# Kernel optimization log

Measured on AMD Instinct MI355X. Metric: run time of the kernel, lower is better.

The kernel has to match this reference:

```python
import jax, jax.numpy as jnp
import numpy as np

EPS = 1e-6

def _mlp3(x, Wa, ba, Wb, bb, Wc, bc):
    h = jax.nn.relu(x @ Wa + ba)
    h = jax.nn.relu(h @ Wb + bb)
    return h @ Wc + bc

def setup_inputs() -> dict:
    key = jax.random.key(0)
    ks = jax.random.split(key, 16)
    B, D, C, N = 1024, 1024, 128, 100000
    s = 0.02  # weight scale
    return {
        "query": jax.random.normal(ks[0], (B, D), jnp.float32),
        "W1": jax.random.normal(ks[1], (D, D // 2), jnp.float32) * s,
        "b1": jnp.zeros((D // 2,), jnp.float32),
        "W2": jax.random.normal(ks[2], (D // 2, D // 4), jnp.float32) * s,
        "b2": jnp.zeros((D // 4,), jnp.float32),
        "W3": jax.random.normal(ks[3], (D // 4, C), jnp.float32) * s,
        "b3": jnp.zeros((C,), jnp.float32),
        "keys": jax.random.normal(ks[4], (N, C), jnp.float32),
        "values": jax.random.normal(ks[5], (N, C), jnp.float32),
        "D1w": jax.random.normal(ks[6], (C, D // 4), jnp.float32) * s,
        "D1b": jnp.zeros((D // 4,), jnp.float32),
        "D2w": jax.random.normal(ks[7], (D // 4, D // 2), jnp.float32) * s,
        "D2b": jnp.zeros((D // 2,), jnp.float32),
        "D3w": jax.random.normal(ks[8], (D // 2, D), jnp.float32) * s,
        "D3b": jnp.zeros((D,), jnp.float32),
        "k": 5,
    }

def reference(query, W1, b1, W2, b2, W3, b3, keys, values,
              D1w, D1b, D2w, D2b, D3w, D3b, k):
    # Compress query (FAISS path detaches, so stop_gradient is faithful)
    cq = _mlp3(query, W1, b1, W2, b2, W3, b3)          # [B, C]
    cq = jax.lax.stop_gradient(cq)
    keys_c = jax.lax.stop_gradient(keys)
    vals = jax.lax.stop_gradient(values)               # stored values were .detach()ed
    # Brute-force squared-L2 distances (IndexFlatL2 returns squared L2): [B, N]
    d2 = (jnp.sum(cq * cq, axis=1, keepdims=True)
          + jnp.sum(keys_c * keys_c, axis=1)[None, :]
          - 2.0 * cq @ keys_c.T)
    neg_d, idx = jax.lax.top_k(-d2, k)                 # k nearest, ascending distance
    dist = -neg_d                                      # [B, k]
    w = 1.0 / (dist + EPS)
    w = w / jnp.sum(w, axis=1, keepdims=True)          # [B, k]
    gathered = vals[idx]                               # [B, k, C]
    weighted = jnp.einsum('bk,bkc->bc', w, gathered)   # [B, C]
    retrieved = _mlp3(weighted, D1w, D1b, D2w, D2b, D3w, D3b)  # [B, D]
    confidence = 1.0 / (dist[:, 0] + EPS)              # [B]
    return retrieved, confidence
```

## Files before the change

### kernel.cpp

```cpp
#include <hip/hip_runtime.h>
#include <hip/hip_bf16.h>

#define NKEYS  100000
#define NCH    128
#define CHK    832
#define TPC    13
#define KPAD   (NCH * CHK)
#define NTILE  (KPAD / 64)
#define BQ     1024
#define EPS_F  1e-6f
#define NCAND  (NCH * 3)
#define BIGF   1e30f

typedef __attribute__((ext_vector_type(8))) short bf16x8;
typedef __attribute__((ext_vector_type(4))) float f32x4;

__device__ __forceinline__ void gl_lds16(const uint4* g, uint4* l) {
    __builtin_amdgcn_global_load_lds((const __attribute__((address_space(1))) void*)g,
                                     (__attribute__((address_space(3))) void*)l, 16, 0, 0);
}
__device__ __forceinline__ unsigned umn(unsigned a, unsigned b) { return a < b ? a : b; }
__device__ __forceinline__ unsigned umx(unsigned a, unsigned b) { return a > b ? a : b; }
__device__ __forceinline__ ushort bf16bits(float v) {
    __hip_bfloat16 h = __float2bfloat16(v);
    return *(ushort*)&h;
}

__device__ __forceinline__ void ins3u(unsigned (&m)[3], unsigned u) {
    unsigned v1 = umn(m[2], u);
    m[2] = umx(m[1], v1);
    unsigned v2 = umn(m[1], v1);
    m[1] = umx(m[0], v2);
    m[0] = umn(m[0], v2);
}

__device__ __forceinline__ void ins5(float (&d)[5], int (&ix)[5], float nd, int ni) {
    if (nd < d[4]) {
        d[4] = nd; ix[4] = ni;
#pragma unroll
        for (int p = 4; p > 0; --p) {
            if (d[p] < d[p - 1]) {
                float td = d[p]; d[p] = d[p - 1]; d[p - 1] = td;
                int   ti = ix[p]; ix[p] = ix[p - 1]; ix[p - 1] = ti;
            }
        }
    }
}

__device__ __forceinline__ void wT_panel(const float* __restrict__ W, uint4* __restrict__ Wimg,
                                         int K, int N, int ctile, int p) {
    const int npan = K >> 6;
#pragma unroll
    for (int it = 0; it < 2; ++it) {
        int c = it * 256 + threadIdx.x;
        int l15 = c & 15, quad = (c >> 4) & 3, s = (c >> 6) & 1, ct = c >> 7;
        int n = ctile * 64 + ct * 16 + l15;
        int k = p * 64 + s * 32 + quad * 8;
        ushort h[8];
#pragma unroll
        for (int j = 0; j < 8; ++j) h[j] = bf16bits(W[(size_t)(k + j) * N + n]);
        Wimg[((size_t)ctile * npan + p) * 512 + c] =
            make_uint4((uint)h[0] | ((uint)h[1] << 16), (uint)h[2] | ((uint)h[3] << 16),
                       (uint)h[4] | ((uint)h[5] << 16), (uint)h[6] | ((uint)h[7] << 16));
    }
}

__global__ __launch_bounds__(256)
void cvt_keys_w(const float* __restrict__ keys, uint4* __restrict__ img,
                float* __restrict__ kk, float* __restrict__ khalf,
                const float* __restrict__ D1w, const float* __restrict__ D2w,
                const float* __restrict__ D3w, uint4* __restrict__ I1,
                uint4* __restrict__ I2, uint4* __restrict__ I3) {
    if (blockIdx.x >= NTILE) {
        int b = blockIdx.x - NTILE;
        if (b < 8)       { wT_panel(D1w, I1, 128, 256,  b >> 1, b & 1); }
        else if (b < 40) { b -= 8;  wT_panel(D2w, I2, 256, 512,  b >> 2, b & 3); }
        else             { b -= 40; wT_panel(D3w, I3, 512, 1024, b >> 3, b & 7); }
        return;
    }
    const int tid = threadIdx.x;
    const int r = tid >> 2, s = tid & 3;
    const int tile = blockIdx.x;
    const int n = tile * 64 + r;
    const int ct = r >> 4, l15 = r & 15;
    const bool live = (n < NKEYS);
    const float* kp = keys + (size_t)n * 128 + s * 32;
    float ss = 0.f;
    uint4 out[4];
#pragma unroll
    for (int q = 0; q < 4; ++q) {
        float4 a = make_float4(0.f, 0.f, 0.f, 0.f), b = a;
        if (live) { a = *(const float4*)(kp + q * 8); b = *(const float4*)(kp + q * 8 + 4); }
        ss += a.x * a.x + a.y * a.y + a.z * a.z + a.w * a.w
            + b.x * b.x + b.y * b.y + b.z * b.z + b.w * b.w;
        float v[8] = {a.x, a.y, a.z, a.w, b.x, b.y, b.z, b.w};
        ushort h[8];
#pragma unroll
        for (int j = 0; j < 8; ++j) h[j] = bf16bits(v[j]);
        out[q] = make_uint4((uint)h[0] | ((uint)h[1] << 16), (uint)h[2] | ((uint)h[3] << 16),
                            (uint)h[4] | ((uint)h[5] << 16), (uint)h[6] | ((uint)h[7] << 16));
    }
    ss += __shfl_xor(ss, 1, 64);
    ss += __shfl_xor(ss, 2, 64);
    if (s == 0) {
        kk[n]    = live ? ss : BIGF;
        khalf[n] = live ? -0.5f * ss : -BIGF;
    }
#pragma unroll
    for (int q = 0; q < 4; ++q)
        img[(size_t)tile * 1024 + ((ct * 4 + s) * 4 + q) * 16 + l15] = out[q];
}

__global__ __launch_bounds__(256)
void prep(const float* __restrict__ A, ushort* __restrict__ Ax,
          const float* __restrict__ W, uint4* __restrict__ Wimg) {
    const int b = blockIdx.x;
    if (b < 1024) {
        const int row = b;
        const int i = threadIdx.x * 4;
        float4 v = *(const float4*)&A[(size_t)row * 1024 + i];
        float x[4] = {v.x, v.y, v.z, v.w};
        ushort h[4], l[4];
#pragma unroll
        for (int j = 0; j < 4; ++j) {
            __hip_bfloat16 hb = __float2bfloat16(x[j]);
            h[j] = *(ushort*)&hb;
            l[j] = bf16bits(x[j] - __bfloat162float(hb));
        }
        ushort* o = Ax + (size_t)row * 3072;
        *(ushort4*)&o[i]        = make_ushort4(h[0], h[1], h[2], h[3]);
        *(ushort4*)&o[1024 + i] = make_ushort4(l[0], l[1], l[2], l[3]);
        *(ushort4*)&o[2048 + i] = make_ushort4(h[0], h[1], h[2], h[3]);
    } else {
        const int idx = b - 1024;
        const int ctile = idx / 48, p = idx % 48;
        const int part = p >> 4, psrc = p & 15;
#pragma unroll
        for (int it = 0; it < 2; ++it) {
            int c = it * 256 + threadIdx.x;
            int l15 = c & 15, quad = (c >> 4) & 3, s = (c >> 6) & 1, ct = c >> 7;
            int n = ctile * 64 + ct * 16 + l15;
            int k = psrc * 64 + s * 32 + quad * 8;
            ushort h[8];
#pragma unroll
            for (int j = 0; j < 8; ++j) {
                float w = W[(size_t)(k + j) * 512 + n];
                __hip_bfloat16 hb = __float2bfloat16(w);
                if (part < 2) h[j] = *(ushort*)&hb;
                else h[j] = bf16bits(w - __bfloat162float(hb));
            }
            Wimg[((size_t)ctile * 48 + p) * 512 + c] =
                make_uint4((uint)h[0] | ((uint)h[1] << 16), (uint)h[2] | ((uint)h[3] << 16),
                           (uint)h[4] | ((uint)h[5] << 16), (uint)h[6] | ((uint)h[7] << 16));
        }
    }
}

__global__ __launch_bounds__(256)
void bgemm_part(const ushort* __restrict__ Abf, const uint4* __restrict__ Wimg,
                float* __restrict__ P, int M, int N, int K, int ppz) {
    __shared__ uint4 pan[2][512];
    const int tid = threadIdx.x;
    const int wv = tid >> 6, ln = tid & 63;
    const int quad = ln >> 4, l15 = ln & 15;
    const int n0 = blockIdx.x * 64;
    const int m0 = blockIdx.y * 128 + wv * 32;
    const int ctile = blockIdx.x, npanT = K >> 6;
    const int p0 = blockIdx.z * ppz;
    f32x4 acc[2][4];
#pragma unroll
    for (int s = 0; s < 2; ++s)
#pragma unroll
        for (int c = 0; c < 4; ++c) acc[s][c] = (f32x4){0.f, 0.f, 0.f, 0.f};

#pragma unroll
    for (int it = 0; it < 2; ++it)
        gl_lds16(&Wimg[((size_t)ctile * npanT + p0) * 512 + it * 256 + wv * 64 + ln],
                 &pan[0][it * 256 + wv * 64]);
    __syncthreads();

    for (int pp = 0; pp < ppz; ++pp) {
        const int p = p0 + pp;
        const int b = pp & 1;
        if (pp + 1 < ppz) {
#pragma unroll
            for (int it = 0; it < 2; ++it)
                gl_lds16(&Wimg[((size_t)ctile * npanT + p + 1) * 512 + it * 256 + wv * 64 + ln],
                         &pan[b ^ 1][it * 256 + wv * 64]);
        }
        const ushort* arow = Abf + (size_t)(m0 + l15) * K + p * 64 + quad * 8;
        bf16x8 afA[2], afB[2];
#pragma unroll
        for (int s = 0; s < 2; ++s) {
            afA[s] = *(const bf16x8*)(arow + s * 32);
            afB[s] = *(const bf16x8*)(arow + (size_t)16 * K + s * 32);
        }
#pragma unroll
        for (int ct = 0; ct < 4; ++ct)
#pragma unroll
            for (int s = 0; s < 2; ++s) {
                bf16x8 bfr = *(const bf16x8*)&pan[b][((ct * 2 + s) * 4 + quad) * 16 + l15];
                acc[0][ct] = __builtin_amdgcn_mfma_f32_16x16x32_bf16(afA[s], bfr, acc[0][ct], 0, 0, 0);
                acc[1][ct] = __builtin_amdgcn_mfma_f32_16x16x32_bf16(afB[s], bfr, acc[1][ct], 0, 0, 0);
            }
        __syncthreads();
    }

    P += (size_t)blockIdx.z * M * N;
#pragma unroll
    for (int ct = 0; ct < 4; ++ct) {
        const int col = n0 + ct * 16 + l15;
#pragma unroll
        for (int set = 0; set < 2; ++set)
#pragma unroll
            for (int r = 0; r < 4; ++r)
                P[(size_t)(m0 + set * 16 + quad * 4 + r) * N + col] = acc[set][ct][r];
    }
}

template <int NP>
__global__ __launch_bounds__(256)
void sgemm_part(const float* __restrict__ A, const float* __restrict__ abias,
                const float* __restrict__ W, float* __restrict__ P,
                int M, int N, int K, int kslice, int MNpart) {
    __shared__ float As[16][68];
    __shared__ float Bs[16][64];
    const int tid = threadIdx.x;
    const int tx = tid & 15, ty = tid >> 4;
    const int m0 = blockIdx.y * 64, n0 = blockIdx.x * 64;
    const int kb = blockIdx.z * kslice, ke = kb + kslice;
    float acc[4][4] = {};
    for (int k0 = kb; k0 < ke; k0 += 16) {
        {
            int m = tid >> 2, k4 = (tid & 3) * 4;
            const float* ap = &A[(size_t)(m0 + m) * K + k0 + k4];
            float4 a = *(const float4*)ap;
            if (NP > 0) {
#pragma unroll
                for (int z = 1; z < NP; ++z) {
                    float4 v = *(const float4*)(ap + (size_t)z * MNpart);
                    a.x += v.x; a.y += v.y; a.z += v.z; a.w += v.w;
                }
                float4 b = *(const float4*)&abias[k0 + k4];
                a.x = fmaxf(a.x + b.x, 0.f); a.y = fmaxf(a.y + b.y, 0.f);
                a.z = fmaxf(a.z + b.z, 0.f); a.w = fmaxf(a.w + b.w, 0.f);
            }
            As[k4 + 0][m] = a.x; As[k4 + 1][m] = a.y;
            As[k4 + 2][m] = a.z; As[k4 + 3][m] = a.w;
        }
        {
            int k = tid >> 4, n4 = (tid & 15) * 4;
            *(float4*)&Bs[k][n4] = *(const float4*)&W[(size_t)(k0 + k) * N + n0 + n4];
        }
        __syncthreads();
#pragma unroll
        for (int kkk = 0; kkk < 16; ++kkk) {
            float4 a4 = *(const float4*)&As[kkk][ty * 4];
            float4 b4 = *(const float4*)&Bs[kkk][tx * 4];
            float av[4] = {a4.x, a4.y, a4.z, a4.w};
            float bv[4] = {b4.x, b4.y, b4.z, b4.w};
#pragma unroll
            for (int i = 0; i < 4; ++i)
#pragma unroll
                for (int j = 0; j < 4; ++j)
                    acc[i][j] = fmaf(av[i], bv[j], acc[i][j]);
        }
        __syncthreads();
    }
    P += (size_t)blockIdx.z * M * N;
#pragma unroll
    for (int i = 0; i < 4; ++i)
        *(float4*)&P[(size_t)(m0 + ty * 4 + i) * N + n0 + tx * 4] =
            make_float4(acc[i][0], acc[i][1], acc[i][2], acc[i][3]);
}

__global__ __launch_bounds__(128)
void layer3_full(const float* __restrict__ partB, const float* __restrict__ b2,
                 const float* __restrict__ W3, const float* __restrict__ b3,
                 float* __restrict__ cq, ushort* __restrict__ qbf,
                 float* __restrict__ qq) {
    __shared__ float h2s[256];
    __shared__ float red[2];
    const int row = blockIdx.x, c = threadIdx.x;
#pragma unroll
    for (int u = 0; u < 2; ++u) {
        const int k = c + u * 128;
        float v = 0.f;
#pragma unroll
        for (int z = 0; z < 4; ++z) v += partB[(size_t)z * (BQ * 256) + row * 256 + k];
        h2s[k] = fmaxf(v + b2[k], 0.f);
    }
    __syncthreads();
    float a0 = 0.f, a1 = 0.f, a2 = 0.f, a3 = 0.f;
#pragma unroll 4
    for (int k = 0; k < 256; k += 4) {
        a0 = fmaf(h2s[k + 0], W3[(size_t)(k + 0) * 128 + c], a0);
        a1 = fmaf(h2s[k + 1], W3[(size_t)(k + 1) * 128 + c], a1);
        a2 = fmaf(h2s[k + 2], W3[(size_t)(k + 2) * 128 + c], a2);
        a3 = fmaf(h2s[k + 3], W3[(size_t)(k + 3) * 128 + c], a3);
    }
    const float out = (a0 + a1) + (a2 + a3) + b3[c];
    cq[(size_t)row * 128 + c] = out;
    qbf[(size_t)row * 128 + c] = bf16bits(out);
    float s = out * out;
#pragma unroll
    for (int off = 32; off > 0; off >>= 1) s += __shfl_down(s, off, 64);
    if ((c & 63) == 0) red[c >> 6] = s;
    __syncthreads();
    if (c == 0) qq[row] = red[0] + red[1];
}

__global__ __launch_bounds__(512, 4)
void screen_topk(const ushort* __restrict__ qbf, const uint4* __restrict__ img,
                 const float* __restrict__ khalf, int* __restrict__ cand_i) {
    __shared__ uint4 buf[2][1024];
    __shared__ float kls[CHK];
    const int tid = threadIdx.x;
    const int wv = tid >> 6, ln = tid & 63;
    const int quad = ln >> 4, l15 = ln & 15;
    const int m0 = blockIdx.y * 256 + wv * 32;
    const int c0 = blockIdx.x * CHK;
    const int t0 = blockIdx.x * TPC;

    bf16x8 afA[4], afB[4];
    {
        const ushort* qa = qbf + (size_t)(m0 + l15) * 128 + quad * 8;
#pragma unroll
        for (int s = 0; s < 4; ++s) {
            afA[s] = *(const bf16x8*)(qa + 32 * s);
            afB[s] = *(const bf16x8*)(qa + 16 * 128 + 32 * s);
        }
    }
    for (int i = tid; i < CHK; i += 512) kls[i] = khalf[c0 + i];

    unsigned mA[4][3], mB[4][3];
#pragma unroll
    for (int r = 0; r < 4; ++r)
#pragma unroll
        for (int p = 0; p < 3; ++p) { mA[r][p] = 0xFFFFFFFFu; mB[r][p] = 0xFFFFFFFFu; }

#pragma unroll
    for (int it = 0; it < 2; ++it)
        gl_lds16(&img[(size_t)t0 * 1024 + it * 512 + wv * 64 + ln],
                 &buf[0][it * 512 + wv * 64]);
    __syncthreads();

    for (int t = 0; t < TPC; ++t) {
        const int b = t & 1;
        if (t + 1 < TPC) {
#pragma unroll
            for (int it = 0; it < 2; ++it)
                gl_lds16(&img[(size_t)(t0 + t + 1) * 1024 + it * 512 + wv * 64 + ln],
                         &buf[b ^ 1][it * 512 + wv * 64]);
        }
#pragma unroll
        for (int ct = 0; ct < 4; ++ct) {
            const int nl = t * 64 + ct * 16 + l15;
            const float kh = kls[nl];
            f32x4 a0 = {kh, kh, kh, kh}, a1 = {kh, kh, kh, kh};
#pragma unroll
            for (int s = 0; s < 4; ++s) {
                bf16x8 bfr = *(const bf16x8*)&buf[b][(ct * 4 + s) * 64 + ln];
                a0 = __builtin_amdgcn_mfma_f32_16x16x32_bf16(afA[s], bfr, a0, 0, 0, 0);
                a1 = __builtin_amdgcn_mfma_f32_16x16x32_bf16(afB[s], bfr, a1, 0, 0, 0);
            }
#pragma unroll
            for (int r = 0; r < 4; ++r) {
                ins3u(mA[r], (__float_as_uint(a0[r]) & 0xFFFFF800u) | (unsigned)nl);
                ins3u(mB[r], (__float_as_uint(a1[r]) & 0xFFFFF800u) | (unsigned)nl);
            }
        }
        __syncthreads();
    }

#pragma unroll
    for (int set = 0; set < 2; ++set) {
#pragma unroll
        for (int r = 0; r < 4; ++r) {
            unsigned m[3];
#pragma unroll
            for (int p = 0; p < 3; ++p) m[p] = set ? mB[r][p] : mA[r][p];
#pragma unroll
            for (int st = 1; st <= 8; st <<= 1) {
                unsigned o[3];
#pragma unroll
                for (int p = 0; p < 3; ++p) o[p] = (unsigned)__shfl_xor((int)m[p], st, 64);
#pragma unroll
                for (int p = 0; p < 3; ++p) ins3u(m, o[p]);
            }
            if (l15 == 0) {
                const int row = m0 + set * 16 + quad * 4 + r;
#pragma unroll
                for (int p = 0; p < 3; ++p)
                    cand_i[((size_t)row * NCH + blockIdx.x) * 3 + p] = c0 + (int)(m[p] & 0x7FFu);
            }
        }
    }
}

__global__ __launch_bounds__(512)
void rerank_gather(const int* __restrict__ cand_i, const float* __restrict__ cq,
                   const float* __restrict__ keysf, const float* __restrict__ qq,
                   const float* __restrict__ kk, const float* __restrict__ values,
                   ushort* __restrict__ wbf, float* __restrict__ conf_out) {
    __shared__ __align__(16) float qs[128];
    __shared__ float ed[NCAND];
    __shared__ int   ei[NCAND];
    __shared__ float w5[5];
    __shared__ int   s5[5];
    __shared__ float confs;
    const int row = blockIdx.x, tid = threadIdx.x;
    const int ln = tid & 63;
    const int qd = tid >> 4;
    const int l15 = tid & 15;
    if (tid < 128) qs[tid] = cq[(size_t)row * 128 + tid];
    for (int c = tid; c < NCAND; c += 512) ei[c] = cand_i[(size_t)row * NCAND + c];
    __syncthreads();
    const float4 qa = *(const float4*)&qs[l15 * 8];
    const float4 qb = *(const float4*)&qs[l15 * 8 + 4];
    const float qqr = qq[row];
#pragma unroll 3
    for (int it = 0; it < (NCAND + 31) / 32; ++it) {
        const int c = qd + it * 32;
        if (c < NCAND) {
            const int idx = ei[c];
            const int idc = idx < NKEYS ? idx : NKEYS - 1;
            const float* kp = &keysf[(size_t)idc * 128 + l15 * 8];
            const float4 ka = *(const float4*)kp;
            const float4 kb = *(const float4*)(kp + 4);
            float dot = qa.x * ka.x + qa.y * ka.y + qa.z * ka.z + qa.w * ka.w
                      + qb.x * kb.x + qb.y * kb.y + qb.z * kb.z + qb.w * kb.w;
            dot += __shfl_xor(dot, 1, 64);
            dot += __shfl_xor(dot, 2, 64);
            dot += __shfl_xor(dot, 4, 64);
            dot += __shfl_xor(dot, 8, 64);
            if (l15 == 0) ed[c] = qqr + kk[idx] - 2.0f * dot;
        }
    }
    __syncthreads();
    if (tid < 64) {
        float bd[5]; int bi[5];
#pragma unroll
        for (int p = 0; p < 5; ++p) { bd[p] = BIGF; bi[p] = 0; }
        for (int c = ln; c < NCAND; c += 64) ins5(bd, bi, ed[c], ei[c]);
#pragma unroll
        for (int m = 1; m <= 32; m <<= 1) {
            float od[5]; int oi[5];
#pragma unroll
            for (int p = 0; p < 5; ++p) {
                od[p] = __shfl_xor(bd[p], m, 64);
                oi[p] = __shfl_xor(bi[p], m, 64);
            }
#pragma unroll
            for (int p = 0; p < 5; ++p) ins5(bd, bi, od[p], oi[p]);
        }
        if (ln == 0) {
            float ww[5]; float s = 0.f;
#pragma unroll
            for (int p = 0; p < 5; ++p) { ww[p] = 1.0f / (bd[p] + EPS_F); s += ww[p]; }
#pragma unroll
            for (int p = 0; p < 5; ++p) { w5[p] = ww[p] / s; s5[p] = bi[p]; }
            confs = 1.0f / (bd[0] + EPS_F);
        }
    }
    __syncthreads();
    if (tid < 128) {
        float acc = 0.f;
#pragma unroll
        for (int p = 0; p < 5; ++p) acc += w5[p] * values[(size_t)s5[p] * 128 + tid];
        wbf[(size_t)row * 128 + tid] = bf16bits(acc);
    }
    if (tid == 0) conf_out[row] = confs;
}

template <int RELU, int OUTF32>
__global__ __launch_bounds__(256)
void bgemm_bias(const ushort* __restrict__ Abf, const uint4* __restrict__ Wimg,
                const float* __restrict__ bias, void* __restrict__ Cout,
                int M, int N, int K) {
    __shared__ uint4 pan[2][512];
    const int tid = threadIdx.x;
    const int wv = tid >> 6, ln = tid & 63;
    const int quad = ln >> 4, l15 = ln & 15;
    const int n0 = blockIdx.x * 64;
    const int m0 = blockIdx.y * 128 + wv * 32;
    const int ctile = blockIdx.x, npan = K >> 6;
    f32x4 acc[2][4];
#pragma unroll
    for (int s = 0; s < 2; ++s)
#pragma unroll
        for (int c = 0; c < 4; ++c) acc[s][c] = (f32x4){0.f, 0.f, 0.f, 0.f};

#pragma unroll
    for (int it = 0; it < 2; ++it)
        gl_lds16(&Wimg[(size_t)ctile * npan * 512 + it * 256 + wv * 64 + ln],
                 &pan[0][it * 256 + wv * 64]);
    __syncthreads();

    for (int p = 0; p < npan; ++p) {
        const int b = p & 1;
        if (p + 1 < npan) {
#pragma unroll
            for (int it = 0; it < 2; ++it)
                gl_lds16(&Wimg[((size_t)ctile * npan + p + 1) * 512 + it * 256 + wv * 64 + ln],
                         &pan[b ^ 1][it * 256 + wv * 64]);
        }
        const ushort* arow = Abf + (size_t)(m0 + l15) * K + p * 64 + quad * 8;
        bf16x8 afA[2], afB[2];
#pragma unroll
        for (int s = 0; s < 2; ++s) {
            afA[s] = *(const bf16x8*)(arow + s * 32);
            afB[s] = *(const bf16x8*)(arow + (size_t)16 * K + s * 32);
        }
#pragma unroll
        for (int ct = 0; ct < 4; ++ct)
#pragma unroll
            for (int s = 0; s < 2; ++s) {
                bf16x8 bfr = *(const bf16x8*)&pan[b][((ct * 2 + s) * 4 + quad) * 16 + l15];
                acc[0][ct] = __builtin_amdgcn_mfma_f32_16x16x32_bf16(afA[s], bfr, acc[0][ct], 0, 0, 0);
                acc[1][ct] = __builtin_amdgcn_mfma_f32_16x16x32_bf16(afB[s], bfr, acc[1][ct], 0, 0, 0);
            }
        __syncthreads();
    }

#pragma unroll
    for (int ct = 0; ct < 4; ++ct) {
        const int col = n0 + ct * 16 + l15;
        const float bv = bias[col];
#pragma unroll
        for (int set = 0; set < 2; ++set)
#pragma unroll
            for (int r = 0; r < 4; ++r) {
                float v = acc[set][ct][r] + bv;
                if (RELU) v = fmaxf(v, 0.f);
                const int row = m0 + set * 16 + quad * 4 + r;
                if (OUTF32) ((float*)Cout)[(size_t)row * N + col] = v;
                else        ((ushort*)Cout)[(size_t)row * N + col] = bf16bits(v);
            }
    }
}

extern "C" void kernel_launch(void* const* d_in, const int* in_sizes, int n_in,
                              void* d_out, int out_size, void* d_ws, size_t ws_size,
                              hipStream_t stream) {
    const float* query  = (const float*)d_in[0];
    const float* W1     = (const float*)d_in[1];
    const float* b1     = (const float*)d_in[2];
    const float* W2     = (const float*)d_in[3];
    const float* b2     = (const float*)d_in[4];
    const float* W3     = (const float*)d_in[5];
    const float* b3     = (const float*)d_in[6];
    const float* keys   = (const float*)d_in[7];
    const float* values = (const float*)d_in[8];
    const float* D1w    = (const float*)d_in[9];
    const float* D1b    = (const float*)d_in[10];
    const float* D2w    = (const float*)d_in[11];
    const float* D2b    = (const float*)d_in[12];
    const float* D3w    = (const float*)d_in[13];
    const float* D3b    = (const float*)d_in[14];
    float* out = (float*)d_out;

    float*  ws    = (float*)d_ws;
    float*  kk    = ws;
    float*  khalf = ws + 106496;
    float*  qq    = ws + 212992;
    float*  cq    = ws + 214016;
    ushort* qbf   = (ushort*)(ws + 345088);
    int*    cand  = (int*)(ws + 410624);
    uint4*  Wimg1 = (uint4*)(ws + 803840);
    uint4*  Wimg2 = (uint4*)(ws + 820224);
    uint4*  Wimg3 = (uint4*)(ws + 885760);
    float*  R     = ws + 1147904;
    ushort* xbig  = (ushort*)R;
    uint4*  W1img = (uint4*)(R + 1572864);
    float*  partA = R + 2359296;
    float*  partB = R + 5505024;
    uint4*  img   = (uint4*)R;
    ushort* wbf   = (ushort*)R;
    ushort* h3bf  = (ushort*)(R + 65536);
    ushort* h4bf  = (ushort*)(R + 196608);
    float*  conf  = out + 1024 * 1024;

    prep<<<1408, 256, 0, stream>>>(query, xbig, W1, W1img);
    bgemm_part<<<dim3(8, 8, 6), 256, 0, stream>>>(xbig, W1img, partA, 1024, 512, 3072, 8);
    sgemm_part<6><<<dim3(4, 16, 4), 256, 0, stream>>>(partA, b1, W2, partB, 1024, 256, 512, 128, 1024 * 512);
    layer3_full<<<1024, 128, 0, stream>>>(partB, b2, W3, b3, cq, qbf, qq);
    cvt_keys_w<<<NTILE + 168, 256, 0, stream>>>(keys, img, kk, khalf,
                                                D1w, D2w, D3w, Wimg1, Wimg2, Wimg3);
    screen_topk<<<dim3(NCH, BQ / 256), 512, 0, stream>>>(qbf, img, khalf, cand);
    rerank_gather<<<BQ, 512, 0, stream>>>(cand, cq, keys, qq, kk, values, wbf, conf);
    bgemm_bias<1, 0><<<dim3(4, 8),  256, 0, stream>>>(wbf,  Wimg1, D1b, h3bf, 1024, 256,  128);
    bgemm_bias<1, 0><<<dim3(8, 8),  256, 0, stream>>>(h3bf, Wimg2, D2b, h4bf, 1024, 512,  256);
    bgemm_bias<0, 1><<<dim3(16, 8), 256, 0, stream>>>(h4bf, Wimg3, D3b, out,  1024, 1024, 512);

    (void)in_sizes; (void)n_in; (void)out_size; (void)ws_size;
}
```

Before: 283.3 us.

## Rebalance screen_topk to 64 rows per wave and shrink decoder GEMM row tiles

screen_topk now runs 256 threads per block, with each wave owning 64 query rows (4 MFMA sets) instead of 32. Each key fragment read from LDS is reused across twice as many MFMAs, which cuts LDS traffic per MFMA, but each thread holds more top-3 registers and occupancy may drop. The decoder bgemm_bias kernels move the other way: each wave computes 16 rows instead of 32, giving twice as many blocks to fill more CUs on these small GEMMs, at the cost of less reuse of the weight panel.

Result: no change. 284.1 us (+0.3%).

```diff
diff --git a/kernel.cpp b/kernel.cpp
--- a/kernel.cpp
+++ b/kernel.cpp
@@ -310,7 +310,7 @@
     if (c == 0) qq[row] = red[0] + red[1];
 }
 
-__global__ __launch_bounds__(512, 4)
+__global__ __launch_bounds__(256)
 void screen_topk(const ushort* __restrict__ qbf, const uint4* __restrict__ img,
                  const float* __restrict__ khalf, int* __restrict__ cand_i) {
     __shared__ uint4 buf[2][1024];
@@ -318,68 +318,71 @@
     const int tid = threadIdx.x;
     const int wv = tid >> 6, ln = tid & 63;
     const int quad = ln >> 4, l15 = ln & 15;
-    const int m0 = blockIdx.y * 256 + wv * 32;
+    const int m0 = blockIdx.y * 256 + wv * 64;
     const int c0 = blockIdx.x * CHK;
     const int t0 = blockIdx.x * TPC;
 
-    bf16x8 afA[4], afB[4];
-    {
-        const ushort* qa = qbf + (size_t)(m0 + l15) * 128 + quad * 8;
-#pragma unroll
-        for (int s = 0; s < 4; ++s) {
-            afA[s] = *(const bf16x8*)(qa + 32 * s);
-            afB[s] = *(const bf16x8*)(qa + 16 * 128 + 32 * s);
-        }
-    }
-    for (int i = tid; i < CHK; i += 512) kls[i] = khalf[c0 + i];
-
-    unsigned mA[4][3], mB[4][3];
-#pragma unroll
-    for (int r = 0; r < 4; ++r)
-#pragma unroll
-        for (int p = 0; p < 3; ++p) { mA[r][p] = 0xFFFFFFFFu; mB[r][p] = 0xFFFFFFFFu; }
-
-#pragma unroll
-    for (int it = 0; it < 2; ++it)
-        gl_lds16(&img[(size_t)t0 * 1024 + it * 512 + wv * 64 + ln],
-                 &buf[0][it * 512 + wv * 64]);
+    bf16x8 af[4][4];
+#pragma unroll
+    for (int set = 0; set < 4; ++set) {
+        const ushort* qa = qbf + (size_t)(m0 + set * 16 + l15) * 128 + quad * 8;
+#pragma unroll
+        for (int s = 0; s < 4; ++s) af[set][s] = *(const bf16x8*)(qa + 32 * s);
+    }
+    for (int i = tid; i < CHK; i += 256) kls[i] = khalf[c0 + i];
+
+    unsigned mm[4][4][3];
+#pragma unroll
+    for (int set = 0; set < 4; ++set)
+#pragma unroll
+        for (int r = 0; r < 4; ++r)
+#pragma unroll
+            for (int p = 0; p < 3; ++p) mm[set][r][p] = 0xFFFFFFFFu;
+
+#pragma unroll
+    for (int it = 0; it < 4; ++it)
+        gl_lds16(&img[(size_t)t0 * 1024 + it * 256 + wv * 64 + ln],
+                 &buf[0][it * 256 + wv * 64]);
     __syncthreads();
 
     for (int t = 0; t < TPC; ++t) {
         const int b = t & 1;
         if (t + 1 < TPC) {
 #pragma unroll
-            for (int it = 0; it < 2; ++it)
-                gl_lds16(&img[(size_t)(t0 + t + 1) * 1024 + it * 512 + wv * 64 + ln],
-                         &buf[b ^ 1][it * 512 + wv * 64]);
+            for (int it = 0; it < 4; ++it)
+                gl_lds16(&img[(size_t)(t0 + t + 1) * 1024 + it * 256 + wv * 64 + ln],
+                         &buf[b ^ 1][it * 256 + wv * 64]);
         }
 #pragma unroll
         for (int ct = 0; ct < 4; ++ct) {
             const int nl = t * 64 + ct * 16 + l15;
             const float kh = kls[nl];
-            f32x4 a0 = {kh, kh, kh, kh}, a1 = {kh, kh, kh, kh};
+            f32x4 a[4];
+#pragma unroll
+            for (int set = 0; set < 4; ++set) a[set] = (f32x4){kh, kh, kh, kh};
 #pragma unroll
             for (int s = 0; s < 4; ++s) {
                 bf16x8 bfr = *(const bf16x8*)&buf[b][(ct * 4 + s) * 64 + ln];
-                a0 = __builtin_amdgcn_mfma_f32_16x16x32_bf16(afA[s], bfr, a0, 0, 0, 0);
-                a1 = __builtin_amdgcn_mfma_f32_16x16x32_bf16(afB[s], bfr, a1, 0, 0, 0);
-            }
-#pragma unroll
-            for (int r = 0; r < 4; ++r) {
-                ins3u(mA[r], (__float_as_uint(a0[r]) & 0xFFFFF800u) | (unsigned)nl);
-                ins3u(mB[r], (__float_as_uint(a1[r]) & 0xFFFFF800u) | (unsigned)nl);
-            }
+#pragma unroll
+                for (int set = 0; set < 4; ++set)
+                    a[set] = __builtin_amdgcn_mfma_f32_16x16x32_bf16(af[set][s], bfr, a[set], 0, 0, 0);
+            }
+#pragma unroll
+            for (int set = 0; set < 4; ++set)
+#pragma unroll
+                for (int r = 0; r < 4; ++r)
+                    ins3u(mm[set][r], (__float_as_uint(a[set][r]) & 0xFFFFF800u) | (unsigned)nl);
         }
         __syncthreads();
     }
 
 #pragma unroll
-    for (int set = 0; set < 2; ++set) {
+    for (int set = 0; set < 4; ++set) {
 #pragma unroll
         for (int r = 0; r < 4; ++r) {
             unsigned m[3];
 #pragma unroll
-            for (int p = 0; p < 3; ++p) m[p] = set ? mB[r][p] : mA[r][p];
+            for (int p = 0; p < 3; ++p) m[p] = mm[set][r][p];
 #pragma unroll
             for (int st = 1; st <= 8; st <<= 1) {
                 unsigned o[3];
@@ -483,13 +486,11 @@
     const int wv = tid >> 6, ln = tid & 63;
     const int quad = ln >> 4, l15 = ln & 15;
     const int n0 = blockIdx.x * 64;
-    const int m0 = blockIdx.y * 128 + wv * 32;
+    const int m0 = blockIdx.y * 64 + wv * 16;
     const int ctile = blockIdx.x, npan = K >> 6;
-    f32x4 acc[2][4];
-#pragma unroll
-    for (int s = 0; s < 2; ++s)
-#pragma unroll
-        for (int c = 0; c < 4; ++c) acc[s][c] = (f32x4){0.f, 0.f, 0.f, 0.f};
+    f32x4 acc[4];
+#pragma unroll
+    for (int c = 0; c < 4; ++c) acc[c] = (f32x4){0.f, 0.f, 0.f, 0.f};
 
 #pragma unroll
     for (int it = 0; it < 2; ++it)
@@ -506,19 +507,15 @@
                          &pan[b ^ 1][it * 256 + wv * 64]);
         }
         const ushort* arow = Abf + (size_t)(m0 + l15) * K + p * 64 + quad * 8;
-        bf16x8 afA[2], afB[2];
-#pragma unroll
-        for (int s = 0; s < 2; ++s) {
-            afA[s] = *(const bf16x8*)(arow + s * 32);
-            afB[s] = *(const bf16x8*)(arow + (size_t)16 * K + s * 32);
-        }
+        bf16x8 afA[2];
+#pragma unroll
+        for (int s = 0; s < 2; ++s) afA[s] = *(const bf16x8*)(arow + s * 32);
 #pragma unroll
         for (int ct = 0; ct < 4; ++ct)
 #pragma unroll
             for (int s = 0; s < 2; ++s) {
                 bf16x8 bfr = *(const bf16x8*)&pan[b][((ct * 2 + s) * 4 + quad) * 16 + l15];
-                acc[0][ct] = __builtin_amdgcn_mfma_f32_16x16x32_bf16(afA[s], bfr, acc[0][ct], 0, 0, 0);
-                acc[1][ct] = __builtin_amdgcn_mfma_f32_16x16x32_bf16(afB[s], bfr, acc[1][ct], 0, 0, 0);
+                acc[ct] = __builtin_amdgcn_mfma_f32_16x16x32_bf16(afA[s], bfr, acc[ct], 0, 0, 0);
             }
         __syncthreads();
     }
@@ -528,15 +525,13 @@
         const int col = n0 + ct * 16 + l15;
         const float bv = bias[col];
 #pragma unroll
-        for (int set = 0; set < 2; ++set)
-#pragma unroll
-            for (int r = 0; r < 4; ++r) {
-                float v = acc[set][ct][r] + bv;
-                if (RELU) v = fmaxf(v, 0.f);
-                const int row = m0 + set * 16 + quad * 4 + r;
-                if (OUTF32) ((float*)Cout)[(size_t)row * N + col] = v;
-                else        ((ushort*)Cout)[(size_t)row * N + col] = bf16bits(v);
-            }
+        for (int r = 0; r < 4; ++r) {
+            float v = acc[ct][r] + bv;
+            if (RELU) v = fmaxf(v, 0.f);
+            const int row = m0 + quad * 4 + r;
+            if (OUTF32) ((float*)Cout)[(size_t)row * N + col] = v;
+            else        ((ushort*)Cout)[(size_t)row * N + col] = bf16bits(v);
+        }
     }
 }
 
@@ -587,11 +582,11 @@
     layer3_full<<<1024, 128, 0, stream>>>(partB, b2, W3, b3, cq, qbf, qq);
     cvt_keys_w<<<NTILE + 168, 256, 0, stream>>>(keys, img, kk, khalf,
                                                 D1w, D2w, D3w, Wimg1, Wimg2, Wimg3);
-    screen_topk<<<dim3(NCH, BQ / 256), 512, 0, stream>>>(qbf, img, khalf, cand);
+    screen_topk<<<dim3(NCH, BQ / 256), 256, 0, stream>>>(qbf, img, khalf, cand);
     rerank_gather<<<BQ, 512, 0, stream>>>(cand, cq, keys, qq, kk, values, wbf, conf);
-    bgemm_bias<1, 0><<<dim3(4, 8),  256, 0, stream>>>(wbf,  Wimg1, D1b, h3bf, 1024, 256,  128);
-    bgemm_bias<1, 0><<<dim3(8, 8),  256, 0, stream>>>(h3bf, Wimg2, D2b, h4bf, 1024, 512,  256);
-    bgemm_bias<0, 1><<<dim3(16, 8), 256, 0, stream>>>(h4bf, Wimg3, D3b, out,  1024, 1024, 512);
+    bgemm_bias<1, 0><<<dim3(4, 16),  256, 0, stream>>>(wbf,  Wimg1, D1b, h3bf, 1024, 256,  128);
+    bgemm_bias<1, 0><<<dim3(8, 16),  256, 0, stream>>>(h3bf, Wimg2, D2b, h4bf, 1024, 512,  256);
+    bgemm_bias<0, 1><<<dim3(16, 16), 256, 0, stream>>>(h4bf, Wimg3, D3b, out,  1024, 1024, 512);
 
     (void)in_sizes; (void)n_in; (void)out_size; (void)ws_size;
 }
```
